# Optimization experiments

Measured on AMD Instinct MI355X. Metric: run time of the kernel, lower is better.

The kernel has to match this reference:

```python
import jax, jax.numpy as jnp
import numpy as np

U, I, J = 256, 512, 31          # nframes, n_actions, atom_max+1
E_IN, N_EMB, N_FIT = 3, 10, 32  # len(elements)+1, N_emb, N_fit
K = N_EMB // 4                  # slice size in the descriptor einsum


def setup_inputs() -> dict:
    key = jax.random.key(0)
    ks = jax.random.split(key, 12)
    s = 0.1
    return {
        "Sg": jax.random.normal(ks[0], (U, I, J, E_IN), jnp.float32),
        "R": jax.random.normal(ks[1], (U, I, J, 4), jnp.float32),
        # mlp_emb: Linear(3,10) -> ReLU -> Linear(10,10)  (weights stored [in,out])
        "W_emb1": jax.random.normal(ks[2], (E_IN, N_EMB), jnp.float32) * s,
        "b_emb1": jax.random.normal(ks[3], (N_EMB,), jnp.float32) * s,
        "W_emb2": jax.random.normal(ks[4], (N_EMB, N_EMB), jnp.float32) * s,
        "b_emb2": jax.random.normal(ks[5], (N_EMB,), jnp.float32) * s,
        # mlp_fit: Linear(20,32) -> ReLU -> Linear(32,32) -> ReLU -> Linear(32,1)
        "W_fit1": jax.random.normal(ks[6], (K * N_EMB, N_FIT), jnp.float32) * s,
        "b_fit1": jax.random.normal(ks[7], (N_FIT,), jnp.float32) * s,
        "W_fit2": jax.random.normal(ks[8], (N_FIT, N_FIT), jnp.float32) * s,
        "b_fit2": jax.random.normal(ks[9], (N_FIT,), jnp.float32) * s,
        "W_fit3": jax.random.normal(ks[10], (N_FIT, 1), jnp.float32) * s,
        "b_fit3": jax.random.normal(ks[11], (1,), jnp.float32) * s,
    }


def reference(Sg, R, W_emb1, b_emb1, W_emb2, b_emb2,
              W_fit1, b_fit1, W_fit2, b_fit2, W_fit3, b_fit3):
    # Embedding MLP on per-neighbor species/weight vectors: [u,i,j,3] -> [u,i,j,10]
    h = jnp.maximum(Sg @ W_emb1 + b_emb1, 0.0)
    Gmat = h @ W_emb2 + b_emb2
    # Descriptor: einsum('uijk,uijl,uiml,uimn->uikn') decomposed to avoid
    # materializing the full 4-way product; sums over both neighbor dims.
    T1 = jnp.einsum('uijk,uijl->uikl', Gmat[..., :K], R)   # [u,i,2,4]
    T2 = jnp.einsum('uiml,uimn->uiln', R, Gmat)            # [u,i,4,10]
    Dmat = jnp.einsum('uikl,uiln->uikn', T1, T2)           # [u,i,2,10]
    D = Dmat.reshape(U * I, K * N_EMB)
    # Fit MLP -> scalar Q per (frame, action)
    f = jnp.maximum(D @ W_fit1 + b_fit1, 0.0)
    f = jnp.maximum(f @ W_fit2 + b_fit2, 0.0)
    Q = f @ W_fit3 + b_fit3
    return Q.reshape(U, I, 1)
```

## Files before the change

### kernel.cpp

```cpp
#include <hip/hip_runtime.h>

constexpr int J_ = 31;
constexpr int UI = 131072;
constexpr size_t D_BYTES = (size_t)UI * 20 * 4;

constexpr int PPB   = 16;
constexpr int SGB   = PPB * 93 * 4;
constexpr int NBLK1 = UI / PPB;

typedef __attribute__((address_space(1))) const void g1void;
typedef __attribute__((address_space(3))) void s3void;

__device__ __forceinline__ float qsum(float x) {
    int a = __builtin_amdgcn_update_dpp(0, __float_as_int(x), 0xB1, 0xF, 0xF, true);
    x += __int_as_float(a);
    int b = __builtin_amdgcn_update_dpp(0, __float_as_int(x), 0x4E, 0xF, 0xF, true);
    x += __int_as_float(b);
    return x;
}

__global__ __launch_bounds__(64) void dqn_phase1(
    const float* __restrict__ Sg, const float* __restrict__ R,
    const float* __restrict__ W1, const float* __restrict__ b1,
    const float* __restrict__ W2, const float* __restrict__ b2,
    float* __restrict__ Dws)
{
    __shared__ float4 sbuf4[384];
    char* sb = reinterpret_cast<char*>(sbuf4);

    const int tid  = threadIdx.x;
    const int lp   = tid >> 2;
    const int g    = tid & 3;
    const int pair = blockIdx.x * PPB + lp;

    const char* gS = reinterpret_cast<const char*>(Sg) + (size_t)blockIdx.x * SGB;
    #pragma unroll
    for (int r = 0; r < 6; ++r) {
        int byte = r * 1024 + tid * 16;
        if (byte > SGB - 16) byte = SGB - 16;
        __builtin_amdgcn_global_load_lds((g1void*)(gS + byte),
                                         (s3void*)(sb + r * 1024), 16, 0, 0);
    }

    float w10[10], w11[10], w12[10], c1w[10];
    #pragma unroll
    for (int p = 0; p < 10; ++p) {
        w10[p] = W1[p]; w11[p] = W1[10 + p]; w12[p] = W1[20 + p]; c1w[p] = b1[p];
    }

    const float4* rv = reinterpret_cast<const float4*>(R + (size_t)pair * 124);
    float4 rqA = rv[g];
    float4 rqB = rv[4 + g];

    asm volatile("s_waitcnt vmcnt(0)" ::: "memory");
    __builtin_amdgcn_sched_barrier(0);

    const float* sgL = reinterpret_cast<const float*>(sb) + lp * 93;

    float M0[10], M1[10], M2[10], M3[10];
    float4 Rs = {0.f, 0.f, 0.f, 0.f};
    #pragma unroll
    for (int p = 0; p < 10; ++p) { M0[p]=0.f; M1[p]=0.f; M2[p]=0.f; M3[p]=0.f; }

    auto PROC = [&](int j, const float4& r4) {
        float s0 = sgL[j * 3 + 0];
        float s1 = sgL[j * 3 + 1];
        float s2 = sgL[j * 3 + 2];
        #pragma unroll
        for (int p = 0; p < 10; ++p) {
            float t = c1w[p] + s0 * w10[p] + s1 * w11[p] + s2 * w12[p];
            t = t > 0.f ? t : 0.f;
            M0[p] += r4.x * t;
            M1[p] += r4.y * t;
            M2[p] += r4.z * t;
            M3[p] += r4.w * t;
        }
        Rs.x += r4.x; Rs.y += r4.y; Rs.z += r4.z; Rs.w += r4.w;
    };

    #pragma unroll 1
    for (int jb = 0; jb < 16; jb += 8) {
        float4 nA = rv[jb +  8 + g];
        float4 nB = rv[jb + 12 + g];
        PROC(jb + g,     rqA);
        PROC(jb + 4 + g, rqB);
        rqA = nA; rqB = nB;
    }
    {
        float4 nA = rv[24 + g];
        int jt = 28 + g;
        float4 nB = rv[jt < J_ ? jt : (J_ - 1)];
        PROC(16 + g, rqA);
        PROC(20 + g, rqB);
        rqA = nA; rqB = nB;
    }
    PROC(24 + g, rqA);
    {
        float m = (g < 3) ? 1.f : 0.f;
        rqB.x *= m; rqB.y *= m; rqB.z *= m; rqB.w *= m;
        PROC(28 + g, rqB);
    }

    #pragma unroll
    for (int p = 0; p < 10; ++p) {
        M0[p] = qsum(M0[p]); M1[p] = qsum(M1[p]);
        M2[p] = qsum(M2[p]); M3[p] = qsum(M3[p]);
    }
    Rs.x = qsum(Rs.x); Rs.y = qsum(Rs.y); Rs.z = qsum(Rs.z); Rs.w = qsum(Rs.w);

    float Mg[10];
    #pragma unroll
    for (int p = 0; p < 10; ++p)
        Mg[p] = (g == 0) ? M0[p] : (g == 1) ? M1[p] : (g == 2) ? M2[p] : M3[p];
    float Rsg = (g == 0) ? Rs.x : (g == 1) ? Rs.y : (g == 2) ? Rs.z : Rs.w;

    float T2g[10];
    #pragma unroll
    for (int n = 0; n < 10; ++n) T2g[n] = Rsg * b2[n];
    #pragma unroll
    for (int p = 0; p < 10; ++p) {
        float m = Mg[p];
        #pragma unroll
        for (int n = 0; n < 10; ++n) T2g[n] += m * W2[p * 10 + n];
    }

    float D[20];
    #pragma unroll
    for (int k = 0; k < 2; ++k)
        #pragma unroll
        for (int n = 0; n < 10; ++n) D[k * 10 + n] = T2g[k] * T2g[n];
    #pragma unroll
    for (int t = 0; t < 20; ++t) D[t] = qsum(D[t]);

    float* dw = Dws + pair;
    if (g == 0) {
        dw[0 * UI] = D[0];  dw[1 * UI] = D[1];  dw[2 * UI] = D[2];
        dw[3 * UI] = D[3];  dw[4 * UI] = D[4];
    } else if (g == 1) {
        dw[5 * UI] = D[5];  dw[6 * UI] = D[6];  dw[7 * UI] = D[7];
        dw[8 * UI] = D[8];  dw[9 * UI] = D[9];
    } else if (g == 2) {
        dw[10 * UI] = D[10]; dw[11 * UI] = D[11]; dw[12 * UI] = D[12];
        dw[13 * UI] = D[13]; dw[14 * UI] = D[14];
    } else {
        dw[15 * UI] = D[15]; dw[16 * UI] = D[16]; dw[17 * UI] = D[17];
        dw[18 * UI] = D[18]; dw[19 * UI] = D[19];
    }
}

__global__ __launch_bounds__(256) void dqn_phase2(
    const float* __restrict__ Dws,
    const float* __restrict__ Wf1, const float* __restrict__ bf1,
    const float* __restrict__ Wf2, const float* __restrict__ bf2,
    const float* __restrict__ Wf3, const float* __restrict__ bf3,
    float* __restrict__ out)
{
    __shared__ float4 wlds4[448];
    const int tid = threadIdx.x;

    {
        if (tid < 160) wlds4[tid] = reinterpret_cast<const float4*>(Wf1)[tid];
        wlds4[160 + tid] = reinterpret_cast<const float4*>(Wf2)[tid];
        if (tid < 8)       wlds4[416 + tid]        = reinterpret_cast<const float4*>(bf1)[tid];
        else if (tid < 16) wlds4[424 + (tid - 8)]  = reinterpret_cast<const float4*>(bf2)[tid - 8];
        else if (tid < 24) wlds4[432 + (tid - 16)] = reinterpret_cast<const float4*>(Wf3)[tid - 16];
        else if (tid == 24) { reinterpret_cast<float*>(wlds4)[1760] = bf3[0]; }
    }
    __syncthreads();

    const int gt   = blockIdx.x * 256 + tid;
    const int pair = gt >> 2;
    const int g    = gt & 3;

    float D[20];
    #pragma unroll
    for (int t = 0; t < 20; ++t) D[t] = Dws[(size_t)t * UI + pair];

    const float* wl = reinterpret_cast<const float*>(wlds4);

    float F[8];
    {
        const float4* b4 = reinterpret_cast<const float4*>(wl + 1664 + g * 8);
        float4 x = b4[0], y = b4[1];
        F[0]=x.x; F[1]=x.y; F[2]=x.z; F[3]=x.w; F[4]=y.x; F[5]=y.y; F[6]=y.z; F[7]=y.w;
    }
    #pragma unroll
    for (int kk = 0; kk < 20; ++kk) {
        float d = D[kk];
        const float4* w4 = reinterpret_cast<const float4*>(wl + kk * 32 + g * 8);
        float4 wa = w4[0], wb = w4[1];
        F[0] += d * wa.x; F[1] += d * wa.y; F[2] += d * wa.z; F[3] += d * wa.w;
        F[4] += d * wb.x; F[5] += d * wb.y; F[6] += d * wb.z; F[7] += d * wb.w;
    }
    #pragma unroll
    for (int i = 0; i < 8; ++i) F[i] = F[i] > 0.f ? F[i] : 0.f;

    float P[8];
    #pragma unroll
    for (int i = 0; i < 8; ++i) P[i] = __shfl_xor(F[i], 1);
    const bool odd = (g & 1);
    float lo[16];
    #pragma unroll
    for (int i = 0; i < 8; ++i) {
        lo[i]     = odd ? P[i] : F[i];
        lo[8 + i] = odd ? F[i] : P[i];
    }
    float hi[16];
    #pragma unroll
    for (int i = 0; i < 16; ++i) hi[i] = __shfl_xor(lo[i], 2);
    const bool up = (g & 2);
    float f1a[32];
    #pragma unroll
    for (int i = 0; i < 16; ++i) {
        f1a[i]      = up ? hi[i] : lo[i];
        f1a[16 + i] = up ? lo[i] : hi[i];
    }

    float G[8];
    {
        const float4* b4 = reinterpret_cast<const float4*>(wl + 1696 + g * 8);
        float4 x = b4[0], y = b4[1];
        G[0]=x.x; G[1]=x.y; G[2]=x.z; G[3]=x.w; G[4]=y.x; G[5]=y.y; G[6]=y.z; G[7]=y.w;
    }
    #pragma unroll
    for (int kk = 0; kk < 32; ++kk) {
        float d = f1a[kk];
        const float4* w4 = reinterpret_cast<const float4*>(wl + 640 + kk * 32 + g * 8);
        float4 wa = w4[0], wb = w4[1];
        G[0] += d * wa.x; G[1] += d * wa.y; G[2] += d * wa.z; G[3] += d * wa.w;
        G[4] += d * wb.x; G[5] += d * wb.y; G[6] += d * wb.z; G[7] += d * wb.w;
    }
    #pragma unroll
    for (int i = 0; i < 8; ++i) G[i] = G[i] > 0.f ? G[i] : 0.f;

    float qp;
    {
        const float4* w4 = reinterpret_cast<const float4*>(wl + 1728 + g * 8);
        float4 wa = w4[0], wb = w4[1];
        qp = G[0]*wa.x + G[1]*wa.y + G[2]*wa.z + G[3]*wa.w
           + G[4]*wb.x + G[5]*wb.y + G[6]*wb.z + G[7]*wb.w;
    }
    qp += __shfl_xor(qp, 1);
    qp += __shfl_xor(qp, 2);
    float q = qp + wl[1760];

    if (g == 0) out[pair] = q;
}

struct Nb1 { float s0, s1, s2; float4 r; };
__device__ __forceinline__ Nb1 load_nb1(const float* __restrict__ sg,
                                        const float* __restrict__ rr, int j) {
    Nb1 d;
    d.s0 = sg[j * 3 + 0]; d.s1 = sg[j * 3 + 1]; d.s2 = sg[j * 3 + 2];
    d.r = *reinterpret_cast<const float4*>(rr + j * 4);
    return d;
}
__global__ __launch_bounds__(256, 2) void dqn_fused_fb(
    const float* __restrict__ Sg,  const float* __restrict__ R,
    const float* __restrict__ W1,  const float* __restrict__ b1,
    const float* __restrict__ W2,  const float* __restrict__ b2,
    const float* __restrict__ Wf1, const float* __restrict__ bf1,
    const float* __restrict__ Wf2, const float* __restrict__ bf2,
    const float* __restrict__ Wf3, const float* __restrict__ bf3,
    float* __restrict__ out)
{
    const int pair = blockIdx.x * 256 + threadIdx.x;
    const float* sg = Sg + (size_t)pair * (J_ * 3);
    const float* rr = R  + (size_t)pair * (J_ * 4);
    float w1[3][10], c1[10];
    #pragma unroll
    for (int k = 0; k < 3; ++k)
        #pragma unroll
        for (int p = 0; p < 10; ++p) w1[k][p] = W1[k * 10 + p];
    #pragma unroll
    for (int p = 0; p < 10; ++p) c1[p] = b1[p];
    float M[4][10]; float Rs[4] = {0.f,0.f,0.f,0.f};
    #pragma unroll
    for (int l = 0; l < 4; ++l)
        #pragma unroll
        for (int p = 0; p < 10; ++p) M[l][p] = 0.f;
    #pragma unroll 1
    for (int j = 0; j < J_; ++j) {
        Nb1 nb = load_nb1(sg, rr, j);
        float h[10];
        #pragma unroll
        for (int p = 0; p < 10; ++p) {
            float t = c1[p] + nb.s0*w1[0][p] + nb.s1*w1[1][p] + nb.s2*w1[2][p];
            h[p] = t > 0.f ? t : 0.f;
        }
        Rs[0]+=nb.r.x; Rs[1]+=nb.r.y; Rs[2]+=nb.r.z; Rs[3]+=nb.r.w;
        #pragma unroll
        for (int p = 0; p < 10; ++p) {
            M[0][p]+=nb.r.x*h[p]; M[1][p]+=nb.r.y*h[p];
            M[2][p]+=nb.r.z*h[p]; M[3][p]+=nb.r.w*h[p];
        }
    }
    float T2[4][10];
    #pragma unroll
    for (int l = 0; l < 4; ++l)
        #pragma unroll
        for (int n = 0; n < 10; ++n) T2[l][n] = Rs[l] * b2[n];
    #pragma unroll
    for (int p = 0; p < 10; ++p) {
        #pragma unroll
        for (int l = 0; l < 4; ++l) {
            float m = M[l][p];
            #pragma unroll
            for (int n = 0; n < 10; ++n) T2[l][n] += m * W2[p * 10 + n];
        }
    }
    float D[20];
    #pragma unroll
    for (int k = 0; k < 2; ++k)
        #pragma unroll
        for (int n = 0; n < 10; ++n)
            D[k*10+n] = T2[0][k]*T2[0][n] + T2[1][k]*T2[1][n]
                      + T2[2][k]*T2[2][n] + T2[3][k]*T2[3][n];
    float f1[32];
    #pragma unroll
    for (int o = 0; o < 32; ++o) f1[o] = bf1[o];
    #pragma unroll
    for (int kk = 0; kk < 20; ++kk) {
        const float4* wrow = reinterpret_cast<const float4*>(Wf1 + kk * 32);
        float d = D[kk];
        #pragma unroll
        for (int v = 0; v < 8; ++v) {
            float4 w = wrow[v];
            f1[4*v+0]+=d*w.x; f1[4*v+1]+=d*w.y; f1[4*v+2]+=d*w.z; f1[4*v+3]+=d*w.w;
        }
    }
    #pragma unroll
    for (int o = 0; o < 32; ++o) f1[o] = f1[o] > 0.f ? f1[o] : 0.f;
    float f2[32];
    #pragma unroll
    for (int o = 0; o < 32; ++o) f2[o] = bf2[o];
    #pragma unroll
    for (int kk = 0; kk < 32; ++kk) {
        const float4* wrow = reinterpret_cast<const float4*>(Wf2 + kk * 32);
        float d = f1[kk];
        #pragma unroll
        for (int v = 0; v < 8; ++v) {
            float4 w = wrow[v];
            f2[4*v+0]+=d*w.x; f2[4*v+1]+=d*w.y; f2[4*v+2]+=d*w.z; f2[4*v+3]+=d*w.w;
        }
    }
    #pragma unroll
    for (int o = 0; o < 32; ++o) f2[o] = f2[o] > 0.f ? f2[o] : 0.f;
    float q = bf3[0];
    #pragma unroll
    for (int o = 0; o < 32; o += 4) {
        float4 w = *reinterpret_cast<const float4*>(Wf3 + o);
        q += f2[o+0]*w.x + f2[o+1]*w.y + f2[o+2]*w.z + f2[o+3]*w.w;
    }
    out[pair] = q;
}

extern "C" void kernel_launch(void* const* d_in, const int* in_sizes, int n_in,
                              void* d_out, int out_size, void* d_ws, size_t ws_size,
                              hipStream_t stream) {
    const float* Sg  = (const float*)d_in[0];
    const float* R   = (const float*)d_in[1];
    const float* W1  = (const float*)d_in[2];
    const float* b1  = (const float*)d_in[3];
    const float* W2  = (const float*)d_in[4];
    const float* b2  = (const float*)d_in[5];
    const float* Wf1 = (const float*)d_in[6];
    const float* bf1 = (const float*)d_in[7];
    const float* Wf2 = (const float*)d_in[8];
    const float* bf2 = (const float*)d_in[9];
    const float* Wf3 = (const float*)d_in[10];
    const float* bf3 = (const float*)d_in[11];
    float* out = (float*)d_out;

    if (ws_size >= D_BYTES) {
        float* Dws = (float*)d_ws;
        dqn_phase1<<<dim3(NBLK1), dim3(64), 0, stream>>>(
            Sg, R, W1, b1, W2, b2, Dws);
        dqn_phase2<<<dim3((UI * 4) / 256), dim3(256), 0, stream>>>(
            Dws, Wf1, bf1, Wf2, bf2, Wf3, bf3, out);
    } else {
        dqn_fused_fb<<<dim3(UI / 256), dim3(256), 0, stream>>>(
            Sg, R, W1, b1, W2, b2, Wf1, bf1, Wf2, bf2, Wf3, bf3, out);
    }
}
```

Before: 44.47 us.

## Double-buffer Sg staging and prefetch R across four tiles per block

Each phase-1 block now handles four 16-pair tiles instead of one. It uses two LDS buffers so the Sg tile and the R vectors for the next tile load while the current tile is computed. Partial vmcnt waits replace the full drain, so memory latency can overlap the embedding and descriptor arithmetic. In exchange the block count drops by four and LDS per block doubles, which cuts how many waves can be resident per CU. It also holds more R registers live, which may raise register pressure.

```diff
diff --git a/kernel.cpp b/kernel.cpp
--- a/kernel.cpp
+++ b/kernel.cpp
@@ -4,9 +4,11 @@
 constexpr int UI = 131072;
 constexpr size_t D_BYTES = (size_t)UI * 20 * 4;
 
-constexpr int PPB   = 16;
-constexpr int SGB   = PPB * 93 * 4;
-constexpr int NBLK1 = UI / PPB;
+constexpr int PPT   = 16;
+constexpr int TILES = 4;
+constexpr int SGB   = PPT * 93 * 4;
+constexpr int SGPAD = 6144;
+constexpr int NBLK1 = UI / (PPT * TILES);
 
 typedef __attribute__((address_space(1))) const void g1void;
 typedef __attribute__((address_space(3))) void s3void;
@@ -25,22 +27,12 @@
     const float* __restrict__ W2, const float* __restrict__ b2,
     float* __restrict__ Dws)
 {
-    __shared__ float4 sbuf4[384];
+    __shared__ float4 sbuf4[2 * SGPAD / 16];
     char* sb = reinterpret_cast<char*>(sbuf4);
 
-    const int tid  = threadIdx.x;
-    const int lp   = tid >> 2;
-    const int g    = tid & 3;
-    const int pair = blockIdx.x * PPB + lp;
-
-    const char* gS = reinterpret_cast<const char*>(Sg) + (size_t)blockIdx.x * SGB;
-    #pragma unroll
-    for (int r = 0; r < 6; ++r) {
-        int byte = r * 1024 + tid * 16;
-        if (byte > SGB - 16) byte = SGB - 16;
-        __builtin_amdgcn_global_load_lds((g1void*)(gS + byte),
-                                         (s3void*)(sb + r * 1024), 16, 0, 0);
-    }
+    const int tid = threadIdx.x;
+    const int lp  = tid >> 2;
+    const int g   = tid & 3;
 
     float w10[10], w11[10], w12[10], c1w[10];
     #pragma unroll
@@ -48,104 +40,132 @@
         w10[p] = W1[p]; w11[p] = W1[10 + p]; w12[p] = W1[20 + p]; c1w[p] = b1[p];
     }
 
-    const float4* rv = reinterpret_cast<const float4*>(R + (size_t)pair * 124);
-    float4 rqA = rv[g];
-    float4 rqB = rv[4 + g];
+    auto STAGE = [&](int tile, int off) {
+        const char* gS = reinterpret_cast<const char*>(Sg) + (size_t)tile * SGB;
+        #pragma unroll
+        for (int r = 0; r < 6; ++r) {
+            int byte = r * 1024 + tid * 16;
+            if (byte > SGB - 16) byte = SGB - 16;
+            __builtin_amdgcn_global_load_lds((g1void*)(gS + byte),
+                                             (s3void*)(sb + off + r * 1024),
+                                             16, 0, 0);
+        }
+    };
+
+    auto LOADR = [&](int tile, float4& r0, float4& r1, float4& r2, float4& r3,
+                     float4& r4, float4& r5, float4& r6, float4& r7) {
+        const float4* rv = reinterpret_cast<const float4*>(
+            R + (size_t)(tile * PPT + lp) * 124);
+        r0 = rv[g];      r1 = rv[4 + g];  r2 = rv[8 + g];  r3 = rv[12 + g];
+        r4 = rv[16 + g]; r5 = rv[20 + g]; r6 = rv[24 + g];
+        int jt = 28 + g;
+        r7 = rv[jt < J_ ? jt : (J_ - 1)];
+    };
+
+    auto COMPUTE = [&](int off, int tileIdx,
+                       float4 r0, float4 r1, float4 r2, float4 r3,
+                       float4 r4, float4 r5, float4 r6, float4 r7) {
+        const float* sgL = reinterpret_cast<const float*>(sb + off) + lp * 93;
+
+        float M0[10], M1[10], M2[10], M3[10];
+        float4 Rs = {0.f, 0.f, 0.f, 0.f};
+        #pragma unroll
+        for (int p = 0; p < 10; ++p) { M0[p]=0.f; M1[p]=0.f; M2[p]=0.f; M3[p]=0.f; }
+
+        auto PROC = [&](int j, const float4& r4v) {
+            float s0 = sgL[j * 3 + 0];
+            float s1 = sgL[j * 3 + 1];
+            float s2 = sgL[j * 3 + 2];
+            #pragma unroll
+            for (int p = 0; p < 10; ++p) {
+                float t = c1w[p] + s0 * w10[p] + s1 * w11[p] + s2 * w12[p];
+                t = t > 0.f ? t : 0.f;
+                M0[p] += r4v.x * t;
+                M1[p] += r4v.y * t;
+                M2[p] += r4v.z * t;
+                M3[p] += r4v.w * t;
+            }
+            Rs.x += r4v.x; Rs.y += r4v.y; Rs.z += r4v.z; Rs.w += r4v.w;
+        };
+
+        PROC(g,      r0); PROC(4 + g,  r1); PROC(8 + g,  r2); PROC(12 + g, r3);
+        PROC(16 + g, r4); PROC(20 + g, r5); PROC(24 + g, r6);
+        {
+            float m = (g < 3) ? 1.f : 0.f;
+            float4 rm = {r7.x * m, r7.y * m, r7.z * m, r7.w * m};
+            PROC(28 + g, rm);
+        }
+
+        #pragma unroll
+        for (int p = 0; p < 10; ++p) {
+            M0[p] = qsum(M0[p]); M1[p] = qsum(M1[p]);
+            M2[p] = qsum(M2[p]); M3[p] = qsum(M3[p]);
+        }
+        Rs.x = qsum(Rs.x); Rs.y = qsum(Rs.y); Rs.z = qsum(Rs.z); Rs.w = qsum(Rs.w);
+
+        float Mg[10];
+        #pragma unroll
+        for (int p = 0; p < 10; ++p)
+            Mg[p] = (g == 0) ? M0[p] : (g == 1) ? M1[p] : (g == 2) ? M2[p] : M3[p];
+        float Rsg = (g == 0) ? Rs.x : (g == 1) ? Rs.y : (g == 2) ? Rs.z : Rs.w;
+
+        float T2g[10];
+        #pragma unroll
+        for (int n = 0; n < 10; ++n) T2g[n] = Rsg * b2[n];
+        #pragma unroll
+        for (int p = 0; p < 10; ++p) {
+            float m = Mg[p];
+            #pragma unroll
+            for (int n = 0; n < 10; ++n) T2g[n] += m * W2[p * 10 + n];
+        }
+
+        float D[20];
+        #pragma unroll
+        for (int k = 0; k < 2; ++k)
+            #pragma unroll
+            for (int n = 0; n < 10; ++n) D[k * 10 + n] = T2g[k] * T2g[n];
+        #pragma unroll
+        for (int t = 0; t < 20; ++t) D[t] = qsum(D[t]);
+
+        float* dw = Dws + tileIdx * PPT + lp;
+        if (g == 0) {
+            dw[0 * UI] = D[0];  dw[1 * UI] = D[1];  dw[2 * UI] = D[2];
+            dw[3 * UI] = D[3];  dw[4 * UI] = D[4];
+        } else if (g == 1) {
+            dw[5 * UI] = D[5];  dw[6 * UI] = D[6];  dw[7 * UI] = D[7];
+            dw[8 * UI] = D[8];  dw[9 * UI] = D[9];
+        } else if (g == 2) {
+            dw[10 * UI] = D[10]; dw[11 * UI] = D[11]; dw[12 * UI] = D[12];
+            dw[13 * UI] = D[13]; dw[14 * UI] = D[14];
+        } else {
+            dw[15 * UI] = D[15]; dw[16 * UI] = D[16]; dw[17 * UI] = D[17];
+            dw[18 * UI] = D[18]; dw[19 * UI] = D[19];
+        }
+    };
+
+    const int t0 = blockIdx.x * TILES;
+    float4 pA0,pA1,pA2,pA3,pA4,pA5,pA6,pA7;
+    float4 pB0,pB1,pB2,pB3,pB4,pB5,pB6,pB7;
+
+    STAGE(t0 + 0, 0);     LOADR(t0 + 0, pA0,pA1,pA2,pA3,pA4,pA5,pA6,pA7);
+    STAGE(t0 + 1, SGPAD); LOADR(t0 + 1, pB0,pB1,pB2,pB3,pB4,pB5,pB6,pB7);
+    asm volatile("s_waitcnt vmcnt(14)" ::: "memory");
+    __builtin_amdgcn_sched_barrier(0);
+    COMPUTE(0, t0 + 0, pA0,pA1,pA2,pA3,pA4,pA5,pA6,pA7);
+
+    STAGE(t0 + 2, 0);     LOADR(t0 + 2, pA0,pA1,pA2,pA3,pA4,pA5,pA6,pA7);
+    asm volatile("s_waitcnt vmcnt(14)" ::: "memory");
+    __builtin_amdgcn_sched_barrier(0);
+    COMPUTE(SGPAD, t0 + 1, pB0,pB1,pB2,pB3,pB4,pB5,pB6,pB7);
+
+    STAGE(t0 + 3, SGPAD); LOADR(t0 + 3, pB0,pB1,pB2,pB3,pB4,pB5,pB6,pB7);
+    asm volatile("s_waitcnt vmcnt(14)" ::: "memory");
+    __builtin_amdgcn_sched_barrier(0);
+    COMPUTE(0, t0 + 2, pA0,pA1,pA2,pA3,pA4,pA5,pA6,pA7);
 
     asm volatile("s_waitcnt vmcnt(0)" ::: "memory");
     __builtin_amdgcn_sched_barrier(0);
-
-    const float* sgL = reinterpret_cast<const float*>(sb) + lp * 93;
-
-    float M0[10], M1[10], M2[10], M3[10];
-    float4 Rs = {0.f, 0.f, 0.f, 0.f};
-    #pragma unroll
-    for (int p = 0; p < 10; ++p) { M0[p]=0.f; M1[p]=0.f; M2[p]=0.f; M3[p]=0.f; }
-
-    auto PROC = [&](int j, const float4& r4) {
-        float s0 = sgL[j * 3 + 0];
-        float s1 = sgL[j * 3 + 1];
-        float s2 = sgL[j * 3 + 2];
-        #pragma unroll
-        for (int p = 0; p < 10; ++p) {
-            float t = c1w[p] + s0 * w10[p] + s1 * w11[p] + s2 * w12[p];
-            t = t > 0.f ? t : 0.f;
-            M0[p] += r4.x * t;
-            M1[p] += r4.y * t;
-            M2[p] += r4.z * t;
-            M3[p] += r4.w * t;
-        }
-        Rs.x += r4.x; Rs.y += r4.y; Rs.z += r4.z; Rs.w += r4.w;
-    };
-
-    #pragma unroll 1
-    for (int jb = 0; jb < 16; jb += 8) {
-        float4 nA = rv[jb +  8 + g];
-        float4 nB = rv[jb + 12 + g];
-        PROC(jb + g,     rqA);
-        PROC(jb + 4 + g, rqB);
-        rqA = nA; rqB = nB;
-    }
-    {
-        float4 nA = rv[24 + g];
-        int jt = 28 + g;
-        float4 nB = rv[jt < J_ ? jt : (J_ - 1)];
-        PROC(16 + g, rqA);
-        PROC(20 + g, rqB);
-        rqA = nA; rqB = nB;
-    }
-    PROC(24 + g, rqA);
-    {
-        float m = (g < 3) ? 1.f : 0.f;
-        rqB.x *= m; rqB.y *= m; rqB.z *= m; rqB.w *= m;
-        PROC(28 + g, rqB);
-    }
-
-    #pragma unroll
-    for (int p = 0; p < 10; ++p) {
-        M0[p] = qsum(M0[p]); M1[p] = qsum(M1[p]);
-        M2[p] = qsum(M2[p]); M3[p] = qsum(M3[p]);
-    }
-    Rs.x = qsum(Rs.x); Rs.y = qsum(Rs.y); Rs.z = qsum(Rs.z); Rs.w = qsum(Rs.w);
-
-    float Mg[10];
-    #pragma unroll
-    for (int p = 0; p < 10; ++p)
-        Mg[p] = (g == 0) ? M0[p] : (g == 1) ? M1[p] : (g == 2) ? M2[p] : M3[p];
-    float Rsg = (g == 0) ? Rs.x : (g == 1) ? Rs.y : (g == 2) ? Rs.z : Rs.w;
-
-    float T2g[10];
-    #pragma unroll
-    for (int n = 0; n < 10; ++n) T2g[n] = Rsg * b2[n];
-    #pragma unroll
-    for (int p = 0; p < 10; ++p) {
-        float m = Mg[p];
-        #pragma unroll
-        for (int n = 0; n < 10; ++n) T2g[n] += m * W2[p * 10 + n];
-    }
-
-    float D[20];
-    #pragma unroll
-    for (int k = 0; k < 2; ++k)
-        #pragma unroll
-        for (int n = 0; n < 10; ++n) D[k * 10 + n] = T2g[k] * T2g[n];
-    #pragma unroll
-    for (int t = 0; t < 20; ++t) D[t] = qsum(D[t]);
-
-    float* dw = Dws + pair;
-    if (g == 0) {
-        dw[0 * UI] = D[0];  dw[1 * UI] = D[1];  dw[2 * UI] = D[2];
-        dw[3 * UI] = D[3];  dw[4 * UI] = D[4];
-    } else if (g == 1) {
-        dw[5 * UI] = D[5];  dw[6 * UI] = D[6];  dw[7 * UI] = D[7];
-        dw[8 * UI] = D[8];  dw[9 * UI] = D[9];
-    } else if (g == 2) {
-        dw[10 * UI] = D[10]; dw[11 * UI] = D[11]; dw[12 * UI] = D[12];
-        dw[13 * UI] = D[13]; dw[14 * UI] = D[14];
-    } else {
-        dw[15 * UI] = D[15]; dw[16 * UI] = D[16]; dw[17 * UI] = D[17];
-        dw[18 * UI] = D[18]; dw[19 * UI] = D[19];
-    }
+    COMPUTE(SGPAD, t0 + 3, pB0,pB1,pB2,pB3,pB4,pB5,pB6,pB7);
 }
 
 __global__ __launch_bounds__(256) void dqn_phase2(
```

Result: slower. 52.52 us (+18.1%).
